# Kernel optimization log

Measured on AMD Instinct MI355X. Metric: run time of the kernel, lower is better.

Reference implementation:

```python
import jax, jax.numpy as jnp
import numpy as np


def _linear(x, W, b):
    # torch nn.Linear: y = x @ W.T + b, W is [out, in]
    return x @ W.T + b


def _sage_layer(x, edge_index, Ws, bs, Wn, bn):
    # GraphSAGE: mean-aggregate neighbor features via scatter-add, then two linears.
    src, tgt = edge_index[0], edge_index[1]
    N = x.shape[0]
    agg = jax.ops.segment_sum(x[src], tgt, num_segments=N)            # [N, D]
    deg = jax.ops.segment_sum(jnp.ones(src.shape, x.dtype), tgt, num_segments=N)  # [N]
    neighbor_mean = agg / jnp.maximum(deg, 1.0)[:, None]
    return _linear(x, Ws, bs) + _linear(neighbor_mean, Wn, bn)


def setup_inputs() -> dict:
    key = jax.random.key(0)
    ks = jax.random.split(key, 16)
    N, ATTR, H, OUT, E = 50000, 125, 128, 128, 800000
    IN = ATTR + 3
    s = 0.05
    inp = {
        "attr_features": jax.random.normal(ks[0], (N, ATTR), jnp.float32),
        "clustering_coefficient": jax.random.uniform(ks[1], (N, 1), jnp.float32),
        "bidirectional_links_ratio": jax.random.uniform(ks[2], (N, 1), jnp.float32),
        "exist_nodes": jnp.ones((N,), jnp.float32),
        "W_in": s * jax.random.normal(ks[3], (H, IN), jnp.float32),
        "b_in": s * jax.random.normal(ks[4], (H,), jnp.float32),
        "W1_self": s * jax.random.normal(ks[5], (H, H), jnp.float32),
        "b1_self": s * jax.random.normal(ks[6], (H,), jnp.float32),
        "W1_neigh": s * jax.random.normal(ks[7], (H, H), jnp.float32),
        "b1_neigh": s * jax.random.normal(ks[8], (H,), jnp.float32),
        "W2_self": s * jax.random.normal(ks[9], (OUT, H), jnp.float32),
        "b2_self": s * jax.random.normal(ks[10], (OUT,), jnp.float32),
        "W2_neigh": s * jax.random.normal(ks[11], (OUT, H), jnp.float32),
        "b2_neigh": s * jax.random.normal(ks[12], (OUT,), jnp.float32),
        "edge_index": jax.random.randint(ks[13], (2, E), 0, N, jnp.int64),
    }
    return inp


def reference(attr_features, clustering_coefficient, bidirectional_links_ratio,
              exist_nodes, W_in, b_in, W1_self, b1_self, W1_neigh, b1_neigh,
              W2_self, b2_self, W2_neigh, b2_neigh, edge_index):
    exist_col = exist_nodes[:, None]                                   # [N, 1]
    x = jnp.concatenate(
        [attr_features, clustering_coefficient, bidirectional_links_ratio, exist_col],
        axis=1)                                                        # [N, attr_dim+3]
    x = jax.nn.relu(_linear(x, W_in, b_in))                            # dropout=0 -> identity
    x = _sage_layer(x, edge_index, W1_self, b1_self, W1_neigh, b1_neigh)
    x = jax.nn.relu(x)
    x = x * exist_col
    x = _sage_layer(x, edge_index, W2_self, b2_self, W2_neigh, b2_neigh)
    return x * exist_col
```

## Files before the change

kernel.cpp:

```cpp
#include <hip/hip_runtime.h>
#include <hip/hip_bf16.h>

typedef __attribute__((ext_vector_type(8))) short short8;
typedef __attribute__((ext_vector_type(4))) float floatx4;

__device__ inline unsigned short f2bf(float f) {
    unsigned u = __float_as_uint(f);
    u += 0x7fffu + ((u >> 16) & 1u);
    return (unsigned short)(u >> 16);
}


__global__ void prep_weights(const float* __restrict__ w_in, const float* __restrict__ w1s,
                             const float* __restrict__ w1n, const float* __restrict__ w2s,
                             const float* __restrict__ w2n,
                             const float* __restrict__ b_in, const float* __restrict__ b1s,
                             const float* __restrict__ b1n, const float* __restrict__ b2s,
                             const float* __restrict__ b2n,
                             unsigned short* __restrict__ wb, float* __restrict__ biasf) {
    int idx = blockIdx.x * 256 + threadIdx.x;
    if (idx < 5 * 16384) {
        int m = idx >> 14, j = idx & 16383;
        const float* src = (m == 0) ? w_in : (m == 1) ? w1s : (m == 2) ? w1n : (m == 3) ? w2s : w2n;
        wb[idx] = f2bf(src[j]);
    }
    if (idx < 128) {
        biasf[idx]       = b_in[idx];
        biasf[128 + idx] = b1s[idx] + b1n[idx];
        biasf[256 + idx] = b2s[idx] + b2n[idx];
    }
}

__global__ void build_x0(const float* __restrict__ attr, const float* __restrict__ cc,
                         const float* __restrict__ bl, const float* __restrict__ ex,
                         unsigned short* __restrict__ x0, int N, int ATTR) {
    int idx = blockIdx.x * 256 + threadIdx.x;
    if (idx >= N * 128) return;
    int row = idx >> 7, col = idx & 127;
    float v;
    if (col < ATTR)            v = attr[row * ATTR + col];
    else if (col == ATTR)      v = cc[row];
    else if (col == ATTR + 1)  v = bl[row];
    else                       v = ex[row];
    x0[idx] = f2bf(v);
}


__global__ __launch_bounds__(256) void chunk_hist(const int* __restrict__ e,
                                                  int* __restrict__ chunk_count, int E) {
    __shared__ int h[128];
    if (threadIdx.x < 128) h[threadIdx.x] = 0;
    __syncthreads();
    for (int i = blockIdx.x * 256 + threadIdx.x; i < E; i += gridDim.x * 256)
        atomicAdd(&h[e[E + i] >> 9], 1);
    __syncthreads();
    if (threadIdx.x < 128 && h[threadIdx.x])
        atomicAdd(&chunk_count[threadIdx.x], h[threadIdx.x]);
}

__global__ void chunk_scan(const int* __restrict__ chunk_count,
                           int* __restrict__ chunk_base, int* __restrict__ chunk_cursor) {
    __shared__ int s[128];
    int t = threadIdx.x;
    int v = chunk_count[t];
    s[t] = v;
    __syncthreads();
    for (int o = 1; o < 128; o <<= 1) {
        int u = (t >= o) ? s[t - o] : 0;
        __syncthreads();
        s[t] += u;
        __syncthreads();
    }
    int excl = s[t] - v;
    chunk_base[t] = excl;
    chunk_cursor[t] = excl;
}

#define BTILE 4096

__global__ __launch_bounds__(256) void bin_pass(const int* __restrict__ e,
                                                int* __restrict__ chunk_cursor,
                                                unsigned* __restrict__ packed_out,
                                                int E, int ntiles) {
    __shared__ unsigned buf[BTILE];
    __shared__ unsigned sbuf[BTILE];
    __shared__ int hist[128], offs[128], gbase[128], lcur[128];
    int t = threadIdx.x;
    for (int tile = blockIdx.x; tile < ntiles; tile += gridDim.x) {
        int e0 = tile * BTILE;
        int cnt = min(BTILE, E - e0);
        if (t < 128) hist[t] = 0;
        __syncthreads();
        for (int j = t; j < cnt; j += 256) {
            unsigned src = (unsigned)e[e0 + j];
            unsigned tgt = (unsigned)e[E + e0 + j];
            unsigned c = tgt >> 9;
            buf[j] = (c << 25) | (src << 9) | (tgt & 511u);
            atomicAdd(&hist[c], 1);
        }
        __syncthreads();
        if (t < 128) offs[t] = hist[t];
        __syncthreads();
        for (int o = 1; o < 128; o <<= 1) {
            int v = (t < 128 && t >= o) ? offs[t - o] : 0;
            __syncthreads();
            if (t < 128) offs[t] += v;
            __syncthreads();
        }
        if (t < 128) {
            int excl = offs[t] - hist[t];
            offs[t] = excl;
            lcur[t] = excl;
            gbase[t] = (hist[t] > 0) ? atomicAdd(&chunk_cursor[t], hist[t]) : 0;
        }
        __syncthreads();
        for (int j = t; j < cnt; j += 256) {
            unsigned v = buf[j];
            int c = v >> 25;
            int p = atomicAdd(&lcur[c], 1);
            sbuf[p] = v;
        }
        __syncthreads();
        int wv = t >> 6, lane = t & 63;
        for (int c = wv; c < 128; c += 4) {
            int n = hist[c], lo = offs[c], gb = gbase[c];
            for (int j = lane; j < n; j += 64)
                packed_out[gb + j] = sbuf[lo + j];
        }
        __syncthreads();
    }
}

#define CSR_CAP 12288

__global__ __launch_bounds__(256) void chunk_csr(const unsigned* __restrict__ packed,
                                                 const int* __restrict__ chunk_base,
                                                 const int* __restrict__ chunk_cursor,
                                                 int* __restrict__ rows, int* __restrict__ colv,
                                                 int N) {
    __shared__ int hist[512], offs[512], lcnt[512], pp[256];
    __shared__ int sbuf[CSR_CAP];
    int c = blockIdx.x;
    int base = chunk_base[c];
    int cnt = chunk_cursor[c] - base;
    int t = threadIdx.x;
    hist[t] = 0;
    hist[t + 256] = 0;
    __syncthreads();
    for (int j = t; j < cnt; j += 256)
        atomicAdd(&hist[packed[base + j] & 511u], 1);
    __syncthreads();
    int a0 = hist[2 * t], a1 = hist[2 * t + 1];
    pp[t] = a0 + a1;
    __syncthreads();
    for (int o = 1; o < 256; o <<= 1) {
        int v = (t >= o) ? pp[t - o] : 0;
        __syncthreads();
        pp[t] += v;
        __syncthreads();
    }
    int excl = pp[t] - (a0 + a1);
    offs[2 * t] = excl;
    offs[2 * t + 1] = excl + a0;
    lcnt[2 * t] = 0;
    lcnt[2 * t + 1] = 0;
    __syncthreads();
    for (int j = t; j < 512; j += 256) {
        int node = c * 512 + j;
        if (node <= N) rows[node] = base + offs[j];
    }
    if (cnt <= CSR_CAP) {
        for (int j = t; j < cnt; j += 256) {
            unsigned v = packed[base + j];
            int node = v & 511u;
            int p = offs[node] + atomicAdd(&lcnt[node], 1);
            sbuf[p] = (v >> 9) & 0xFFFFu;
        }
        __syncthreads();
        for (int j = t; j < cnt; j += 256) colv[base + j] = sbuf[j];
    } else {
        for (int j = t; j < cnt; j += 256) {
            unsigned v = packed[base + j];
            int node = v & 511u;
            int p = offs[node] + atomicAdd(&lcnt[node], 1);
            colv[base + p] = (v >> 9) & 0xFFFFu;
        }
    }
}


__global__ __launch_bounds__(256) void agg_mean(const unsigned short* __restrict__ x,
                                                const int* __restrict__ rows,
                                                const int* __restrict__ colv,
                                                unsigned short* __restrict__ nm, int N) {
    int wid = (blockIdx.x * 256 + threadIdx.x) >> 6;
    int lane = threadIdx.x & 63;
    if (wid >= N) return;
    int s0 = rows[wid], s1 = rows[wid + 1];
    int deg = s1 - s0;
    int mn = deg < 64 ? deg : 64;
    int cvec = (lane < mn) ? colv[s0 + lane] : 0;
    float a0 = 0.f, a1 = 0.f;
    int lim = mn - 1;
    for (int j = 0; j < mn; j += 8) {
        unsigned v[8];
        #pragma unroll
        for (int u = 0; u < 8; ++u) {
            int idx = (j + u <= lim) ? (j + u) : lim;
            int s = __shfl(cvec, idx, 64);
            v[u] = *(const unsigned*)(x + (size_t)s * 128 + lane * 2);
        }
        #pragma unroll
        for (int u = 0; u < 8; ++u) {
            if (j + u <= lim) {
                a0 += __uint_as_float(v[u] << 16);
                a1 += __uint_as_float(v[u] & 0xffff0000u);
            }
        }
    }
    for (int e = s0 + 64; e < s1; ++e) {
        int s = colv[e];
        unsigned v_ = *(const unsigned*)(x + (size_t)s * 128 + lane * 2);
        a0 += __uint_as_float(v_ << 16);
        a1 += __uint_as_float(v_ & 0xffff0000u);
    }
    float inv = 1.0f / (float)(deg > 1 ? deg : 1);
    a0 *= inv;
    a1 *= inv;
    unsigned outp = ((unsigned)f2bf(a1) << 16) | (unsigned)f2bf(a0);
    *(unsigned*)(nm + (size_t)wid * 128 + lane * 2) = outp;
}


__global__ __launch_bounds__(256, 3) void gemm_fused(
    const unsigned short* __restrict__ X0, const unsigned short* __restrict__ X1,
    const unsigned short* __restrict__ W0, const unsigned short* __restrict__ W1,
    const float* __restrict__ bias, const float* __restrict__ ex,
    unsigned short* __restrict__ obf, float* __restrict__ of32,
    int N, int relu, int nphase) {
    __shared__ unsigned short lx[64 * 136];
    __shared__ unsigned short lw[128 * 136];
    int tid = threadIdx.x;
    int lane = tid & 63;
    int w = tid >> 6;
    int node0 = blockIdx.x * 64;
    int n_off = w * 32;
    int q = lane >> 4;
    int m16 = lane & 15;

    floatx4 acc[4][2];
    for (int nt = 0; nt < 2; ++nt) {
        float bv = bias[n_off + nt * 16 + m16];
        floatx4 b4 = {bv, bv, bv, bv};
        for (int mt = 0; mt < 4; ++mt) acc[mt][nt] = b4;
    }

    for (int ph = 0; ph < nphase; ++ph) {
        const unsigned short* X = ph ? X1 : X0;
        const unsigned short* W = ph ? W1 : W0;
        for (int i = 0; i < 4; ++i) {
            int c = tid + 256 * i;
            int nd = c >> 4, ck = c & 15;
            short8 v = {0, 0, 0, 0, 0, 0, 0, 0};
            if (node0 + nd < N) v = *(const short8*)(X + (size_t)(node0 + nd) * 128 + ck * 8);
            *(short8*)(lx + nd * 136 + ck * 8) = v;
        }
        for (int i = 0; i < 8; ++i) {
            int c = tid + 256 * i;
            int rw = c >> 4, ck = c & 15;
            *(short8*)(lw + rw * 136 + ck * 8) = *(const short8*)(W + rw * 128 + ck * 8);
        }
        __syncthreads();
        for (int kk = 0; kk < 4; ++kk) {
            short8 a[4], b[2];
            for (int mt = 0; mt < 4; ++mt)
                a[mt] = *(const short8*)(lx + (mt * 16 + m16) * 136 + kk * 32 + q * 8);
            for (int nt = 0; nt < 2; ++nt)
                b[nt] = *(const short8*)(lw + (n_off + nt * 16 + m16) * 136 + kk * 32 + q * 8);
            for (int mt = 0; mt < 4; ++mt)
                for (int nt = 0; nt < 2; ++nt)
                    acc[mt][nt] = __builtin_amdgcn_mfma_f32_16x16x32_bf16(a[mt], b[nt], acc[mt][nt], 0, 0, 0);
        }
        __syncthreads();
    }

    for (int mt = 0; mt < 4; ++mt) {
        int rbase = node0 + mt * 16 + q * 4;
        for (int r = 0; r < 4; ++r) {
            int rr = rbase + r;
            if (rr >= N) continue;
            float e = ex ? ex[rr] : 1.0f;
            for (int nt = 0; nt < 2; ++nt) {
                float v = acc[mt][nt][r];
                if (relu) v = fmaxf(v, 0.0f);
                v *= e;
                int col = n_off + nt * 16 + m16;
                if (obf) obf[(size_t)rr * 128 + col] = f2bf(v);
                else     of32[(size_t)rr * 128 + col] = v;
            }
        }
    }
}


extern "C" void kernel_launch(void* const* d_in, const int* in_sizes, int n_in,
                              void* d_out, int out_size, void* d_ws, size_t ws_size,
                              hipStream_t stream) {
    const float* attr = (const float*)d_in[0];
    const float* cc   = (const float*)d_in[1];
    const float* bl   = (const float*)d_in[2];
    const float* ex   = (const float*)d_in[3];
    const float* w_in = (const float*)d_in[4];
    const float* b_in = (const float*)d_in[5];
    const float* w1s  = (const float*)d_in[6];
    const float* b1s  = (const float*)d_in[7];
    const float* w1n  = (const float*)d_in[8];
    const float* b1n  = (const float*)d_in[9];
    const float* w2s  = (const float*)d_in[10];
    const float* b2s  = (const float*)d_in[11];
    const float* w2n  = (const float*)d_in[12];
    const float* b2n  = (const float*)d_in[13];
    const int*   eidx = (const int*)d_in[14];

    int N = in_sizes[3];
    int ATTR = in_sizes[0] / N;
    int E = in_sizes[14] / 2;
    int Npad = ((N + 63) / 64) * 64;
    int nchunk = (N >> 9) + 1;
    int ntiles = (E + BTILE - 1) / BTILE;

    char* ws = (char*)d_ws;
    size_t off = 0;
    auto alloc = [&](size_t bytes) -> char* {
        off = (off + 255) & ~(size_t)255;
        char* p = ws + off;
        off += bytes;
        return p;
    };
    unsigned short* xa = (unsigned short*)alloc((size_t)Npad * 128 * 2);
    unsigned short* xb = (unsigned short*)alloc((size_t)Npad * 128 * 2);
    unsigned short* xc = (unsigned short*)alloc((size_t)Npad * 128 * 2);
    int* colv = (int*)alloc((size_t)E * 4);
    unsigned* packed = (unsigned*)alloc((size_t)E * 4);
    int* rows = (int*)alloc((size_t)(N + 256) * 4);
    int* chunk_count  = (int*)alloc(128 * 4);
    int* chunk_base   = (int*)alloc(128 * 4);
    int* chunk_cursor = (int*)alloc(128 * 4);
    unsigned short* wb = (unsigned short*)alloc((size_t)5 * 16384 * 2);
    float* biasf = (float*)alloc(3 * 128 * 4);

    hipMemsetAsync(chunk_count, 0, 128 * 4, stream);

    prep_weights<<<(5 * 16384 + 255) / 256, 256, 0, stream>>>(
        w_in, w1s, w1n, w2s, w2n, b_in, b1s, b1n, b2s, b2n, wb, biasf);
    build_x0<<<(N * 128 + 255) / 256, 256, 0, stream>>>(attr, cc, bl, ex, xa, N, ATTR);

    chunk_hist<<<256, 256, 0, stream>>>(eidx, chunk_count, E);
    chunk_scan<<<1, 128, 0, stream>>>(chunk_count, chunk_base, chunk_cursor);
    bin_pass<<<(ntiles < 256 ? ntiles : 256), 256, 0, stream>>>(eidx, chunk_cursor, packed, E, ntiles);
    chunk_csr<<<nchunk, 256, 0, stream>>>(packed, chunk_base, chunk_cursor, rows, colv, N);

    int gblk = Npad / 64;
    gemm_fused<<<gblk, 256, 0, stream>>>(xa, (const unsigned short*)nullptr,
                                         wb, (const unsigned short*)nullptr,
                                         biasf, (const float*)nullptr,
                                         xb, (float*)nullptr, N, 1, 1);
    agg_mean<<<(N + 3) / 4, 256, 0, stream>>>(xb, rows, colv, xc, N);
    gemm_fused<<<gblk, 256, 0, stream>>>(xb, xc, wb + 16384, wb + 2 * 16384,
                                         biasf + 128, ex, xa, (float*)nullptr, N, 1, 2);
    agg_mean<<<(N + 3) / 4, 256, 0, stream>>>(xa, rows, colv, xc, N);
    gemm_fused<<<gblk, 256, 0, stream>>>(xa, xc, wb + 3 * 16384, wb + 4 * 16384,
                                         biasf + 256, ex, (unsigned short*)nullptr,
                                         (float*)d_out, N, 0, 2);
}
```

Baseline: 268.0 us.

## Fuse input build into GEMM, merge hist+scan, persistent GEMM with register weights

Drops the build_x0 kernel: the first GEMM now reads the raw fp32 attribute and extra columns and converts them to bf16 while staging its LDS tile. chunk_hist and chunk_scan become one kernel, where the last block (found through an atomic done counter) does the scan, and the memset moves into prep_weights. gemm_fused becomes persistent over two tiles per block, holds the weight fragments in registers loaded once, and loads both phases' activations before one barrier. agg_mean's gather unroll goes from 8 to 16 to keep more loads in flight. Risks are extra register pressure and the last-block-done fence pattern.

Result: slower. 277.8 us (+3.6%).

```diff
diff --git a/kernel.cpp b/kernel.cpp
--- a/kernel.cpp
+++ b/kernel.cpp
@@ -17,7 +17,8 @@
                              const float* __restrict__ b_in, const float* __restrict__ b1s,
                              const float* __restrict__ b1n, const float* __restrict__ b2s,
                              const float* __restrict__ b2n,
-                             unsigned short* __restrict__ wb, float* __restrict__ biasf) {
+                             unsigned short* __restrict__ wb, float* __restrict__ biasf,
+                             int* __restrict__ chunk_count, int* __restrict__ done_ctr) {
     int idx = blockIdx.x * 256 + threadIdx.x;
     if (idx < 5 * 16384) {
         int m = idx >> 14, j = idx & 16383;
@@ -29,51 +30,47 @@
         biasf[128 + idx] = b1s[idx] + b1n[idx];
         biasf[256 + idx] = b2s[idx] + b2n[idx];
     }
-}
-
-__global__ void build_x0(const float* __restrict__ attr, const float* __restrict__ cc,
-                         const float* __restrict__ bl, const float* __restrict__ ex,
-                         unsigned short* __restrict__ x0, int N, int ATTR) {
-    int idx = blockIdx.x * 256 + threadIdx.x;
-    if (idx >= N * 128) return;
-    int row = idx >> 7, col = idx & 127;
-    float v;
-    if (col < ATTR)            v = attr[row * ATTR + col];
-    else if (col == ATTR)      v = cc[row];
-    else if (col == ATTR + 1)  v = bl[row];
-    else                       v = ex[row];
-    x0[idx] = f2bf(v);
+    if (blockIdx.x == 0) {
+        if (threadIdx.x < 128) chunk_count[threadIdx.x] = 0;
+        if (threadIdx.x == 128) *done_ctr = 0;
+    }
 }
 
 
 __global__ __launch_bounds__(256) void chunk_hist(const int* __restrict__ e,
-                                                  int* __restrict__ chunk_count, int E) {
+                                                  int* __restrict__ chunk_count,
+                                                  int* __restrict__ chunk_base,
+                                                  int* __restrict__ chunk_cursor,
+                                                  int* __restrict__ done_ctr,
+                                                  int E, int nblocks) {
     __shared__ int h[128];
-    if (threadIdx.x < 128) h[threadIdx.x] = 0;
-    __syncthreads();
-    for (int i = blockIdx.x * 256 + threadIdx.x; i < E; i += gridDim.x * 256)
+    __shared__ int lastf;
+    int t = threadIdx.x;
+    if (t < 128) h[t] = 0;
+    __syncthreads();
+    for (int i = blockIdx.x * 256 + t; i < E; i += nblocks * 256)
         atomicAdd(&h[e[E + i] >> 9], 1);
     __syncthreads();
-    if (threadIdx.x < 128 && h[threadIdx.x])
-        atomicAdd(&chunk_count[threadIdx.x], h[threadIdx.x]);
-}
-
-__global__ void chunk_scan(const int* __restrict__ chunk_count,
-                           int* __restrict__ chunk_base, int* __restrict__ chunk_cursor) {
-    __shared__ int s[128];
-    int t = threadIdx.x;
-    int v = chunk_count[t];
-    s[t] = v;
-    __syncthreads();
-    for (int o = 1; o < 128; o <<= 1) {
-        int u = (t >= o) ? s[t - o] : 0;
-        __syncthreads();
-        s[t] += u;
-        __syncthreads();
-    }
-    int excl = s[t] - v;
-    chunk_base[t] = excl;
-    chunk_cursor[t] = excl;
+    if (t < 128 && h[t]) atomicAdd(&chunk_count[t], h[t]);
+    __threadfence();
+    if (t == 0) lastf = (atomicAdd(done_ctr, 1) == nblocks - 1);
+    __syncthreads();
+    if (lastf) {
+        int cv = (t < 128) ? atomicAdd(&chunk_count[t], 0) : 0;
+        if (t < 128) h[t] = cv;
+        __syncthreads();
+        for (int o = 1; o < 128; o <<= 1) {
+            int v = (t < 128 && t >= o) ? h[t - o] : 0;
+            __syncthreads();
+            if (t < 128) h[t] += v;
+            __syncthreads();
+        }
+        if (t < 128) {
+            int excl = h[t] - cv;
+            chunk_base[t] = excl;
+            chunk_cursor[t] = excl;
+        }
+    }
 }
 
 #define BTILE 4096
@@ -202,16 +199,16 @@
     int cvec = (lane < mn) ? colv[s0 + lane] : 0;
     float a0 = 0.f, a1 = 0.f;
     int lim = mn - 1;
-    for (int j = 0; j < mn; j += 8) {
-        unsigned v[8];
-        #pragma unroll
-        for (int u = 0; u < 8; ++u) {
+    for (int j = 0; j < mn; j += 16) {
+        unsigned v[16];
+        #pragma unroll
+        for (int u = 0; u < 16; ++u) {
             int idx = (j + u <= lim) ? (j + u) : lim;
             int s = __shfl(cvec, idx, 64);
             v[u] = *(const unsigned*)(x + (size_t)s * 128 + lane * 2);
         }
         #pragma unroll
-        for (int u = 0; u < 8; ++u) {
+        for (int u = 0; u < 16; ++u) {
             if (j + u <= lim) {
                 a0 += __uint_as_float(v[u] << 16);
                 a1 += __uint_as_float(v[u] & 0xffff0000u);
@@ -232,73 +229,157 @@
 }
 
 
+#define LXS 8704
+
 __global__ __launch_bounds__(256, 3) void gemm_fused(
     const unsigned short* __restrict__ X0, const unsigned short* __restrict__ X1,
     const unsigned short* __restrict__ W0, const unsigned short* __restrict__ W1,
     const float* __restrict__ bias, const float* __restrict__ ex,
+    const float* __restrict__ attr, const float* __restrict__ cc,
+    const float* __restrict__ bl, const float* __restrict__ exn,
     unsigned short* __restrict__ obf, float* __restrict__ of32,
-    int N, int relu, int nphase) {
-    __shared__ unsigned short lx[64 * 136];
-    __shared__ unsigned short lw[128 * 136];
+    int N, int ATTR, int relu, int nphase, int raw, int ntile) {
+    __shared__ unsigned short lbuf[2 * LXS];
     int tid = threadIdx.x;
     int lane = tid & 63;
     int w = tid >> 6;
-    int node0 = blockIdx.x * 64;
     int n_off = w * 32;
     int q = lane >> 4;
     int m16 = lane & 15;
 
-    floatx4 acc[4][2];
-    for (int nt = 0; nt < 2; ++nt) {
-        float bv = bias[n_off + nt * 16 + m16];
-        floatx4 b4 = {bv, bv, bv, bv};
-        for (int mt = 0; mt < 4; ++mt) acc[mt][nt] = b4;
-    }
-
-    for (int ph = 0; ph < nphase; ++ph) {
-        const unsigned short* X = ph ? X1 : X0;
-        const unsigned short* W = ph ? W1 : W0;
-        for (int i = 0; i < 4; ++i) {
-            int c = tid + 256 * i;
-            int nd = c >> 4, ck = c & 15;
-            short8 v = {0, 0, 0, 0, 0, 0, 0, 0};
-            if (node0 + nd < N) v = *(const short8*)(X + (size_t)(node0 + nd) * 128 + ck * 8);
-            *(short8*)(lx + nd * 136 + ck * 8) = v;
-        }
+    short8 bf0[2][4], bf1[2][4];
+    {
         for (int i = 0; i < 8; ++i) {
             int c = tid + 256 * i;
             int rw = c >> 4, ck = c & 15;
-            *(short8*)(lw + rw * 136 + ck * 8) = *(const short8*)(W + rw * 128 + ck * 8);
-        }
-        __syncthreads();
+            *(short8*)(lbuf + rw * 136 + ck * 8) = *(const short8*)(W0 + rw * 128 + ck * 8);
+        }
+        __syncthreads();
+        #pragma unroll
+        for (int nt = 0; nt < 2; ++nt)
+            #pragma unroll
+            for (int kk = 0; kk < 4; ++kk)
+                bf0[nt][kk] = *(const short8*)(lbuf + (n_off + nt * 16 + m16) * 136 + kk * 32 + q * 8);
+        __syncthreads();
+        if (nphase == 2) {
+            for (int i = 0; i < 8; ++i) {
+                int c = tid + 256 * i;
+                int rw = c >> 4, ck = c & 15;
+                *(short8*)(lbuf + rw * 136 + ck * 8) = *(const short8*)(W1 + rw * 128 + ck * 8);
+            }
+            __syncthreads();
+            #pragma unroll
+            for (int nt = 0; nt < 2; ++nt)
+                #pragma unroll
+                for (int kk = 0; kk < 4; ++kk)
+                    bf1[nt][kk] = *(const short8*)(lbuf + (n_off + nt * 16 + m16) * 136 + kk * 32 + q * 8);
+            __syncthreads();
+        }
+    }
+    float bv0 = bias[n_off + m16];
+    float bv1 = bias[n_off + 16 + m16];
+
+    for (int tile = blockIdx.x; tile < ntile; tile += gridDim.x) {
+        int node0 = tile * 64;
+        if (raw) {
+            for (int i = 0; i < 4; ++i) {
+                int c = tid + 256 * i;
+                int nd = c >> 4, ck = c & 15;
+                int node = node0 + nd;
+                short8 v = {0, 0, 0, 0, 0, 0, 0, 0};
+                if (node < N) {
+                    if (ck < 15) {
+                        const float* p = attr + (size_t)node * ATTR + ck * 8;
+                        #pragma unroll
+                        for (int u = 0; u < 8; ++u) ((unsigned short*)&v)[u] = f2bf(p[u]);
+                    } else {
+                        #pragma unroll
+                        for (int u = 0; u < 8; ++u) {
+                            int col = 120 + u;
+                            float f = (col < ATTR) ? attr[(size_t)node * ATTR + col]
+                                    : (col == ATTR) ? cc[node]
+                                    : (col == ATTR + 1) ? bl[node] : exn[node];
+                            ((unsigned short*)&v)[u] = f2bf(f);
+                        }
+                    }
+                }
+                *(short8*)(lbuf + nd * 136 + ck * 8) = v;
+            }
+        } else {
+            for (int i = 0; i < 4; ++i) {
+                int c = tid + 256 * i;
+                int nd = c >> 4, ck = c & 15;
+                short8 v = {0, 0, 0, 0, 0, 0, 0, 0};
+                if (node0 + nd < N) v = *(const short8*)(X0 + (size_t)(node0 + nd) * 128 + ck * 8);
+                *(short8*)(lbuf + nd * 136 + ck * 8) = v;
+            }
+        }
+        if (nphase == 2) {
+            for (int i = 0; i < 4; ++i) {
+                int c = tid + 256 * i;
+                int nd = c >> 4, ck = c & 15;
+                short8 v = {0, 0, 0, 0, 0, 0, 0, 0};
+                if (node0 + nd < N) v = *(const short8*)(X1 + (size_t)(node0 + nd) * 128 + ck * 8);
+                *(short8*)(lbuf + LXS + nd * 136 + ck * 8) = v;
+            }
+        }
+        __syncthreads();
+
+        floatx4 acc[4][2];
+        #pragma unroll
+        for (int mt = 0; mt < 4; ++mt) {
+            floatx4 b40 = {bv0, bv0, bv0, bv0};
+            floatx4 b41 = {bv1, bv1, bv1, bv1};
+            acc[mt][0] = b40;
+            acc[mt][1] = b41;
+        }
+        #pragma unroll
         for (int kk = 0; kk < 4; ++kk) {
-            short8 a[4], b[2];
+            short8 a[4];
+            #pragma unroll
             for (int mt = 0; mt < 4; ++mt)
-                a[mt] = *(const short8*)(lx + (mt * 16 + m16) * 136 + kk * 32 + q * 8);
-            for (int nt = 0; nt < 2; ++nt)
-                b[nt] = *(const short8*)(lw + (n_off + nt * 16 + m16) * 136 + kk * 32 + q * 8);
-            for (int mt = 0; mt < 4; ++mt)
-                for (int nt = 0; nt < 2; ++nt)
-                    acc[mt][nt] = __builtin_amdgcn_mfma_f32_16x16x32_bf16(a[mt], b[nt], acc[mt][nt], 0, 0, 0);
-        }
-        __syncthreads();
-    }
-
-    for (int mt = 0; mt < 4; ++mt) {
-        int rbase = node0 + mt * 16 + q * 4;
-        for (int r = 0; r < 4; ++r) {
-            int rr = rbase + r;
-            if (rr >= N) continue;
-            float e = ex ? ex[rr] : 1.0f;
-            for (int nt = 0; nt < 2; ++nt) {
-                float v = acc[mt][nt][r];
-                if (relu) v = fmaxf(v, 0.0f);
-                v *= e;
-                int col = n_off + nt * 16 + m16;
-                if (obf) obf[(size_t)rr * 128 + col] = f2bf(v);
-                else     of32[(size_t)rr * 128 + col] = v;
-            }
-        }
+                a[mt] = *(const short8*)(lbuf + (mt * 16 + m16) * 136 + kk * 32 + q * 8);
+            #pragma unroll
+            for (int mt = 0; mt < 4; ++mt) {
+                acc[mt][0] = __builtin_amdgcn_mfma_f32_16x16x32_bf16(a[mt], bf0[0][kk], acc[mt][0], 0, 0, 0);
+                acc[mt][1] = __builtin_amdgcn_mfma_f32_16x16x32_bf16(a[mt], bf0[1][kk], acc[mt][1], 0, 0, 0);
+            }
+        }
+        if (nphase == 2) {
+            #pragma unroll
+            for (int kk = 0; kk < 4; ++kk) {
+                short8 a[4];
+                #pragma unroll
+                for (int mt = 0; mt < 4; ++mt)
+                    a[mt] = *(const short8*)(lbuf + LXS + (mt * 16 + m16) * 136 + kk * 32 + q * 8);
+                #pragma unroll
+                for (int mt = 0; mt < 4; ++mt) {
+                    acc[mt][0] = __builtin_amdgcn_mfma_f32_16x16x32_bf16(a[mt], bf1[0][kk], acc[mt][0], 0, 0, 0);
+                    acc[mt][1] = __builtin_amdgcn_mfma_f32_16x16x32_bf16(a[mt], bf1[1][kk], acc[mt][1], 0, 0, 0);
+                }
+            }
+        }
+
+        #pragma unroll
+        for (int mt = 0; mt < 4; ++mt) {
+            int rbase = node0 + mt * 16 + q * 4;
+            #pragma unroll
+            for (int r = 0; r < 4; ++r) {
+                int rr = rbase + r;
+                if (rr >= N) continue;
+                float e = ex ? ex[rr] : 1.0f;
+                #pragma unroll
+                for (int nt = 0; nt < 2; ++nt) {
+                    float v = acc[mt][nt][r];
+                    if (relu) v = fmaxf(v, 0.0f);
+                    v *= e;
+                    int col = n_off + nt * 16 + m16;
+                    if (obf) obf[(size_t)rr * 128 + col] = f2bf(v);
+                    else     of32[(size_t)rr * 128 + col] = v;
+                }
+            }
+        }
+        __syncthreads();
     }
 }
 
@@ -327,7 +408,9 @@
     int E = in_sizes[14] / 2;
     int Npad = ((N + 63) / 64) * 64;
     int nchunk = (N >> 9) + 1;
-    int ntiles = (E + BTILE - 1) / BTILE;
+    int ntilesE = (E + BTILE - 1) / BTILE;
+    int ntile = Npad / 64;
+    int gblk = (ntile + 1) / 2;
 
     char* ws = (char*)d_ws;
     size_t off = 0;
@@ -346,30 +429,32 @@
     int* chunk_count  = (int*)alloc(128 * 4);
     int* chunk_base   = (int*)alloc(128 * 4);
     int* chunk_cursor = (int*)alloc(128 * 4);
+    int* done_ctr     = (int*)alloc(4);
     unsigned short* wb = (unsigned short*)alloc((size_t)5 * 16384 * 2);
     float* biasf = (float*)alloc(3 * 128 * 4);
 
-    hipMemsetAsync(chunk_count, 0, 128 * 4, stream);
-
     prep_weights<<<(5 * 16384 + 255) / 256, 256, 0, stream>>>(
-        w_in, w1s, w1n, w2s, w2n, b_in, b1s, b1n, b2s, b2n, wb, biasf);
-    build_x0<<<(N * 128 + 255) / 256, 256, 0, stream>>>(attr, cc, bl, ex, xa, N, ATTR);
-
-    chunk_hist<<<256, 256, 0, stream>>>(eidx, chunk_count, E);
-    chunk_scan<<<1, 128, 0, stream>>>(chunk_count, chunk_base, chunk_cursor);
-    bin_pass<<<(ntiles < 256 ? ntiles : 256), 256, 0, stream>>>(eidx, chunk_cursor, packed, E, ntiles);
+        w_in, w1s, w1n, w2s, w2n, b_in, b1s, b1n, b2s, b2n, wb, biasf,
+        chunk_count, done_ctr);
+
+    chunk_hist<<<256, 256, 0, stream>>>(eidx, chunk_count, chunk_base, chunk_cursor,
+                                        done_ctr, E, 256);
+    bin_pass<<<(ntilesE < 256 ? ntilesE : 256), 256, 0, stream>>>(eidx, chunk_cursor, packed, E, ntilesE);
     chunk_csr<<<nchunk, 256, 0, stream>>>(packed, chunk_base, chunk_cursor, rows, colv, N);
 
-    int gblk = Npad / 64;
-    gemm_fused<<<gblk, 256, 0, stream>>>(xa, (const unsigned short*)nullptr,
+    gemm_fused<<<gblk, 256, 0, stream>>>((const unsigned short*)nullptr, (const unsigned short*)nullptr,
                                          wb, (const unsigned short*)nullptr,
                                          biasf, (const float*)nullptr,
-                                         xb, (float*)nullptr, N, 1, 1);
+                                         attr, cc, bl, ex,
+                                         xb, (float*)nullptr, N, ATTR, 1, 1, 1, ntile);
     agg_mean<<<(N + 3) / 4, 256, 0, stream>>>(xb, rows, colv, xc, N);
     gemm_fused<<<gblk, 256, 0, stream>>>(xb, xc, wb + 16384, wb + 2 * 16384,
-                                         biasf + 128, ex, xa, (float*)nullptr, N, 1, 2);
+                                         biasf + 128, ex,
+                                         attr, cc, bl, ex,
+                                         xa, (float*)nullptr, N, ATTR, 1, 2, 0, ntile);
     agg_mean<<<(N + 3) / 4, 256, 0, stream>>>(xa, rows, colv, xc, N);
     gemm_fused<<<gblk, 256, 0, stream>>>(xa, xc, wb + 3 * 16384, wb + 4 * 16384,
-                                         biasf + 256, ex, (unsigned short*)nullptr,
-                                         (float*)d_out, N, 0, 2);
-}
+                                         biasf + 256, ex,
+                                         attr, cc, bl, ex,
+                                         (unsigned short*)nullptr, (float*)d_out, N, ATTR, 0, 2, 0, ntile);
+}
```
